# Kernel optimization log

Measured on AMD Instinct MI355X. Metric: run time of the kernel, lower is better.

The kernel has to match this reference:

```python
import jax, jax.numpy as jnp
import numpy as np

EMB = 8
HID = 64
B = 1000
T = 512
N = (B * T) // 5  # events per source; sources partition the (batch,time) grid

_KEYS = ["ccba", "cdtx", "cust", "dp", "remit"]
_NUMS = {"ccba": 8, "cdtx": 1, "cust": 1, "dp": 2, "remit": 1}
_CATS = {"ccba": 0, "cdtx": 2, "cust": 3, "dp": 8, "remit": 1}
_VOCAB = {"ccba": 0, "cdtx": 179, "cust": 37, "dp": 435, "remit": 5}


def setup_inputs() -> dict:
    ks = iter(jax.random.split(jax.random.key(0), 64))
    rng = np.random.default_rng(0)
    chunks = np.split(rng.permutation(B * T), 5)
    d = {}
    for k5, ch in zip(_KEYS, chunks):
        d[k5 + "_num"] = jax.random.normal(next(ks), (N, _NUMS[k5]), jnp.float32)
        if _CATS[k5] > 0:
            d[k5 + "_cat"] = jax.random.randint(next(ks), (N, _CATS[k5]), 0, _VOCAB[k5])
            d[k5 + "_tab"] = jax.random.normal(next(ks), (_VOCAB[k5], EMB), jnp.float32) * 0.1
        d[k5 + "_bi"] = jnp.asarray(ch // T, jnp.int32)
        d[k5 + "_ti"] = jnp.asarray(ch % T, jnp.int32)
        in_dim = _CATS[k5] * EMB + _NUMS[k5]
        d[k5 + "_W"] = jax.random.normal(next(ks), (in_dim, HID), jnp.float32) * np.float32(1.0 / np.sqrt(in_dim))
        d[k5 + "_b"] = jnp.zeros((HID,), jnp.float32)
    # LSTM: 2 layers x 2 directions, hidden 64, proj_size 1 -> layer1 input is 2
    for l, insz in [(0, HID), (1, 2)]:
        d[f"Wih{l}"] = jax.random.normal(next(ks), (2, 4 * HID, insz), jnp.float32) * 0.05
        d[f"Whh{l}"] = jax.random.normal(next(ks), (2, 4 * HID, 1), jnp.float32) * 0.05
        d[f"Whr{l}"] = jax.random.normal(next(ks), (2, 1, HID), jnp.float32) * 0.05
        d[f"bih{l}"] = jnp.zeros((2, 4 * HID), jnp.float32)
        d[f"bhh{l}"] = jnp.zeros((2, 4 * HID), jnp.float32)
    d["length"] = T
    d["batch_size"] = B
    return d


def _embed(num, cat, tab, W, b):
    # FeatureEmbedder: concat(categorical embeddings, numeric) -> Linear(hidden)
    x = num if cat is None else jnp.concatenate([tab[cat].reshape(cat.shape[0], -1), num], axis=-1)
    return x @ W + b


def _lstm_dir(x, Wih, Whh, Whr, bih, bhh, reverse):
    Bx = x.shape[0]
    H = Whr.shape[1]
    p = Whr.shape[0]
    bias = bih + bhh

    def step(carry, xt):
        h, c = carry  # h: [B,p] projected hidden, c: [B,H] cell
        g = xt @ Wih.T + h @ Whh.T + bias
        i, f, gg, o = jnp.split(g, 4, axis=-1)  # PyTorch gate order i,f,g,o
        c = jax.nn.sigmoid(f) * c + jax.nn.sigmoid(i) * jnp.tanh(gg)
        h = (jax.nn.sigmoid(o) * jnp.tanh(c)) @ Whr.T  # proj_size projection
        return (h, c), h

    init = (jnp.zeros((Bx, p), x.dtype), jnp.zeros((Bx, H), x.dtype))
    _, ys = jax.lax.scan(step, init, jnp.swapaxes(x, 0, 1), reverse=reverse)
    return jnp.swapaxes(ys, 0, 1)  # [B,T,p]


def _bilstm(x, Wih, Whh, Whr, bih, bhh):
    fwd = _lstm_dir(x, Wih[0], Whh[0], Whr[0], bih[0], bhh[0], False)
    bwd = _lstm_dir(x, Wih[1], Whh[1], Whr[1], bih[1], bhh[1], True)
    return jnp.concatenate([fwd, bwd], axis=-1)


def _forward(a):
    feat = jnp.zeros((a["batch_size"], a["length"], HID), jnp.float32)
    for k5 in _KEYS:
        v = _embed(a[k5 + "_num"], a.get(k5 + "_cat"), a.get(k5 + "_tab"), a[k5 + "_W"], a[k5 + "_b"])
        feat = feat.at[a[k5 + "_bi"], a[k5 + "_ti"]].set(v)  # scatter-assemble padded tensor
    h = _bilstm(feat, a["Wih0"], a["Whh0"], a["Whr0"], a["bih0"], a["bhh0"])
    h = _bilstm(h, a["Wih1"], a["Whh1"], a["Whr1"], a["bih1"], a["bhh1"])
    return h.mean(axis=2)  # [B,T]


def reference(ccba_num, ccba_bi, ccba_ti, ccba_W, ccba_b,
              cdtx_num, cdtx_cat, cdtx_tab, cdtx_bi, cdtx_ti, cdtx_W, cdtx_b,
              cust_num, cust_cat, cust_tab, cust_bi, cust_ti, cust_W, cust_b,
              dp_num, dp_cat, dp_tab, dp_bi, dp_ti, dp_W, dp_b,
              remit_num, remit_cat, remit_tab, remit_bi, remit_ti, remit_W, remit_b,
              Wih0, Whh0, Whr0, bih0, bhh0, Wih1, Whh1, Whr1, bih1, bhh1,
              length, batch_size):
    return _forward(dict(locals()))
```

## Files before the change

### kernel.cpp

```cpp
#include <hip/hip_runtime.h>
#include <cstdint>
#include <cstddef>

#define TLEN 512
#define BATCH 1000
#define NEV 102400
#define HID 64

__device__ __forceinline__ float fast_rcp(float x) {
#if __has_builtin(__builtin_amdgcn_rcpf)
    return __builtin_amdgcn_rcpf(x);
#else
    return 1.0f / x;
#endif
}
__device__ __forceinline__ float sigm(float x) { return fast_rcp(1.0f + __expf(-x)); }
__device__ __forceinline__ float tanh_f(float x) { return fmaf(2.0f, sigm(2.0f * x), -1.0f); }


__global__ __launch_bounds__(512) void compose_kernel(
    const float* __restrict__ W0, const float* __restrict__ B0,
    const float* __restrict__ W1, const float* __restrict__ B1,
    const float* __restrict__ W2, const float* __restrict__ B2,
    const float* __restrict__ W3, const float* __restrict__ B3,
    const float* __restrict__ W4, const float* __restrict__ B4,
    const float* __restrict__ Wih, const float* __restrict__ bih,
    const float* __restrict__ bhh, float* __restrict__ wp)
{
    const int col = threadIdx.x;
    const int row = blockIdx.x;
    const float* srcW; const float* srcB; int base, IND;
    if (row < 9)        { srcW = W0; srcB = B0; base = 0;   IND = 8;  }
    else if (row < 27)  { srcW = W1; srcB = B1; base = 9;   IND = 17; }
    else if (row < 53)  { srcW = W2; srcB = B2; base = 27;  IND = 25; }
    else if (row < 120) { srcW = W3; srcB = B3; base = 53;  IND = 66; }
    else                { srcW = W4; srcB = B4; base = 120; IND = 9;  }
    const int j = row - base;
    const float* xrow = (j < IND) ? (srcW + (size_t)j * 64) : srcB;
    const float* wr = Wih + (size_t)col * 64;
    float acc = 0.0f;
#pragma unroll
    for (int h2 = 0; h2 < 64; ++h2) acc = fmaf(xrow[h2], wr[h2], acc);
    if (j == IND) acc += bih[col] + bhh[col];
    wp[(size_t)row * 512 + col] = acc;
}

template<int NNUM, int NCAT>
__global__ __launch_bounds__(512) void project_kernel(
    const float* __restrict__ num, const int* __restrict__ cat,
    const float* __restrict__ tab, const int* __restrict__ bi,
    const int* __restrict__ ti, const float* __restrict__ wp,
    float* __restrict__ gpre)
{
    constexpr int IND = NCAT * 8 + NNUM;
    const int col = threadIdx.x;
    float wcol[IND];
#pragma unroll
    for (int j = 0; j < IND; ++j) wcol[j] = wp[(size_t)j * 512 + col];
    const float bcol = wp[(size_t)IND * 512 + col];

    for (int ev = blockIdx.x; ev < NEV; ev += gridDim.x) {
        const int pos = bi[ev] * TLEN + ti[ev];
        float acc = bcol;
#pragma unroll
        for (int c0 = 0; c0 < NCAT; ++c0) {
            const int idx = cat[ev * NCAT + c0];
            const float* tr = tab + (size_t)idx * 8;
#pragma unroll
            for (int u = 0; u < 8; ++u)
                acc = fmaf(tr[u], wcol[c0 * 8 + u], acc);
        }
#pragma unroll
        for (int u = 0; u < NNUM; ++u)
            acc = fmaf(num[(size_t)ev * NNUM + u], wcol[NCAT * 8 + u], acc);
        gpre[(size_t)pos * 512 + col] = acc;
    }
}

__global__ __launch_bounds__(256) void rec0_kernel(
    const float* __restrict__ gpre, const float* __restrict__ Whh,
    const float* __restrict__ Whr, float* __restrict__ h0)
{
    const int wv = threadIdx.x >> 6, lane = threadIdx.x & 63;
    const int p = blockIdx.x * 4 + wv;
    const int b = p >> 1, dir = p & 1;

    float whh4[4];
#pragma unroll
    for (int k = 0; k < 4; ++k) whh4[k] = Whh[dir * 256 + k * 64 + lane];
    const float whr = Whr[dir * HID + lane];

    const float* gb = gpre + (size_t)dir * 256 + lane;
    float* h0p = h0 + (size_t)b * TLEN * 2 + dir;

    auto addr = [&](int t) -> const float* {
        int tc = t < TLEN ? t : TLEN - 1;
        int tt = dir ? (TLEN - 1 - tc) : tc;
        return gb + ((size_t)(b * TLEN + tt)) * 512;
    };

    float A[4], B[4];
    {
        const float* pa = addr(0); const float* pb = addr(1);
#pragma unroll
        for (int k = 0; k < 4; ++k) { A[k] = pa[k * 64]; B[k] = pb[k * 64]; }
    }
    float h = 0.0f, c = 0.0f;

    for (int t = 0; t < TLEN; t += 2) {
        float C[4], D[4];
        const float* pc = addr(t + 2); const float* pd = addr(t + 3);
#pragma unroll
        for (int k = 0; k < 4; ++k) { C[k] = pc[k * 64]; D[k] = pd[k * 64]; }

        {
            float gi = fmaf(whh4[0], h, A[0]);
            float gf = fmaf(whh4[1], h, A[1]);
            float gg = fmaf(whh4[2], h, A[2]);
            float go = fmaf(whh4[3], h, A[3]);
            c = sigm(gf) * c + sigm(gi) * tanh_f(gg);
            float pp = sigm(go) * tanh_f(c) * whr;
#pragma unroll
            for (int off = 1; off < 64; off <<= 1) pp += __shfl_xor(pp, off, 64);
            h = pp;
            int tt = dir ? (TLEN - 1 - t) : t;
            if (lane == 0) h0p[(size_t)tt * 2] = h;
        }
        {
            float gi = fmaf(whh4[0], h, B[0]);
            float gf = fmaf(whh4[1], h, B[1]);
            float gg = fmaf(whh4[2], h, B[2]);
            float go = fmaf(whh4[3], h, B[3]);
            c = sigm(gf) * c + sigm(gi) * tanh_f(gg);
            float pp = sigm(go) * tanh_f(c) * whr;
#pragma unroll
            for (int off = 1; off < 64; off <<= 1) pp += __shfl_xor(pp, off, 64);
            h = pp;
            int tt = dir ? (TLEN - 2 - t) : (t + 1);
            if (lane == 0) h0p[(size_t)tt * 2] = h;
        }
#pragma unroll
        for (int k = 0; k < 4; ++k) { A[k] = C[k]; B[k] = D[k]; }
    }
}

__global__ __launch_bounds__(256) void lstm1_kernel(
    const float* __restrict__ h0, const float* __restrict__ Wih,
    const float* __restrict__ Whh, const float* __restrict__ Whr,
    const float* __restrict__ bih, const float* __restrict__ bhh,
    float* __restrict__ h1)
{
    int w = threadIdx.x >> 6, lane = threadIdx.x & 63;
    int p = blockIdx.x * 4 + w;
    int b = p >> 1, dir = p & 1;

    float wi0[4], wi1[4], whh[4], bias[4];
#pragma unroll
    for (int k = 0; k < 4; ++k) {
        int r = k * 64 + lane;
        wi0[k] = Wih[(size_t)(dir * 256 + r) * 2 + 0];
        wi1[k] = Wih[(size_t)(dir * 256 + r) * 2 + 1];
        whh[k] = Whh[dir * 256 + r];
        bias[k] = bih[dir * 256 + r] + bhh[dir * 256 + r];
    }
    float whr = Whr[dir * HID + lane];
    float h = 0.0f, c = 0.0f;
    const float* hb = h0 + (size_t)b * TLEN * 2;

    auto xat = [&](int t) -> float2 {
        int tc = t < TLEN ? t : TLEN - 1;
        int tt = dir ? (TLEN - 1 - tc) : tc;
        return *(const float2*)(hb + (size_t)tt * 2);
    };

    float2 xA = xat(0), xB = xat(1);
    for (int t = 0; t < TLEN; t += 2) {
        float2 xC = xat(t + 2), xD = xat(t + 3);
        {
            float g[4];
#pragma unroll
            for (int k = 0; k < 4; ++k)
                g[k] = fmaf(whh[k], h, fmaf(wi1[k], xA.y, fmaf(wi0[k], xA.x, bias[k])));
            c = sigm(g[1]) * c + sigm(g[0]) * tanh_f(g[2]);
            float pp = sigm(g[3]) * tanh_f(c) * whr;
#pragma unroll
            for (int off = 1; off < 64; off <<= 1) pp += __shfl_xor(pp, off, 64);
            h = pp;
            int tt = dir ? (TLEN - 1 - t) : t;
            if (lane == 0) h1[((size_t)b * TLEN + tt) * 2 + dir] = h;
        }
        {
            float g[4];
#pragma unroll
            for (int k = 0; k < 4; ++k)
                g[k] = fmaf(whh[k], h, fmaf(wi1[k], xB.y, fmaf(wi0[k], xB.x, bias[k])));
            c = sigm(g[1]) * c + sigm(g[0]) * tanh_f(g[2]);
            float pp = sigm(g[3]) * tanh_f(c) * whr;
#pragma unroll
            for (int off = 1; off < 64; off <<= 1) pp += __shfl_xor(pp, off, 64);
            h = pp;
            int tt = dir ? (TLEN - 2 - t) : (t + 1);
            if (lane == 0) h1[((size_t)b * TLEN + tt) * 2 + dir] = h;
        }
        xA = xC; xB = xD;
    }
}

__global__ __launch_bounds__(256) void mean_kernel(
    const float2* __restrict__ h1, float* __restrict__ out)
{
    int i = blockIdx.x * 256 + threadIdx.x;
    if (i < BATCH * TLEN) {
        float2 v = h1[i];
        out[i] = 0.5f * (v.x + v.y);
    }
}

__global__ __launch_bounds__(256) void embed_kernel(
    const float* __restrict__ num, const int* __restrict__ cat,
    const float* __restrict__ tab, const int* __restrict__ bi,
    const int* __restrict__ ti, const float* __restrict__ W,
    const float* __restrict__ bvec, float* __restrict__ feat,
    int n_num, int n_cat)
{
    int e = blockIdx.x * 4 + (threadIdx.x >> 6);
    int hh = threadIdx.x & 63;
    if (e >= NEV) return;
    float acc = bvec[hh];
    int j = 0;
    for (int c = 0; c < n_cat; ++c) {
        int idx = cat[e * n_cat + c];
        const float* trow = tab + (size_t)idx * 8;
#pragma unroll
        for (int u = 0; u < 8; ++u)
            acc = fmaf(trow[u], W[(j + u) * HID + hh], acc);
        j += 8;
    }
    for (int u = 0; u < n_num; ++u)
        acc = fmaf(num[(size_t)e * n_num + u], W[(j + u) * HID + hh], acc);
    int pos = bi[e] * TLEN + ti[e];
    feat[(size_t)pos * HID + hh] = acc;
}

__global__ __launch_bounds__(256, 2) void lstm0_kernel(
    const float* __restrict__ feat, const float* __restrict__ Wih,
    const float* __restrict__ Whh, const float* __restrict__ Whr,
    const float* __restrict__ bih, const float* __restrict__ bhh,
    float* __restrict__ h0)
{
    const int b0 = blockIdx.x * 4;
    const int dir = blockIdx.y;
    const int tid = threadIdx.x, lane = tid & 63, wv = tid >> 6;

    const float* wrow = Wih + (size_t)(dir * 256 + tid) * HID;
    float4 w[16];
#pragma unroll
    for (int i = 0; i < 16; ++i) w[i] = ((const float4*)wrow)[i];
    const float whh = Whh[dir * 256 + tid];
    const float bias = bih[dir * 256 + tid] + bhh[dir * 256 + tid];
    const float whr = Whr[dir * HID + lane];

    __shared__ float4 featb[2][4][16];
    __shared__ float gbuf[4][256];
    __shared__ __align__(16) float hbuf[4];

    float c = 0.0f;
    const float* fb = feat + (size_t)(b0 + wv) * TLEN * HID;
    float* h0b = h0 + ((size_t)(b0 + wv) * TLEN) * 2 + dir;

    const int t0 = dir ? (TLEN - 1) : 0;
    ((float*)featb[0][wv])[lane] = fb[(size_t)t0 * HID + lane];
    if (tid < 4) hbuf[tid] = 0.0f;
    __syncthreads();

    for (int t = 0; t < TLEN; ++t) {
        const int buf = t & 1;
        const int tt = dir ? (TLEN - 1 - t) : t;
        float nf = 0.0f;
        const int tn = dir ? (TLEN - 2 - t) : (t + 1);
        const bool pf = (t < TLEN - 1);
        if (pf) nf = fb[(size_t)tn * HID + lane];
        const float4 hp = *(const float4*)hbuf;
        float a0 = fmaf(whh, hp.x, bias);
        float a1 = fmaf(whh, hp.y, bias);
        float a2 = fmaf(whh, hp.z, bias);
        float a3 = fmaf(whh, hp.w, bias);
#pragma unroll
        for (int i = 0; i < 16; ++i) {
            float4 f0 = featb[buf][0][i];
            float4 f1 = featb[buf][1][i];
            float4 f2 = featb[buf][2][i];
            float4 f3 = featb[buf][3][i];
            a0 = fmaf(f0.x, w[i].x, a0); a0 = fmaf(f0.y, w[i].y, a0);
            a0 = fmaf(f0.z, w[i].z, a0); a0 = fmaf(f0.w, w[i].w, a0);
            a1 = fmaf(f1.x, w[i].x, a1); a1 = fmaf(f1.y, w[i].y, a1);
            a1 = fmaf(f1.z, w[i].z, a1); a1 = fmaf(f1.w, w[i].w, a1);
            a2 = fmaf(f2.x, w[i].x, a2); a2 = fmaf(f2.y, w[i].y, a2);
            a2 = fmaf(f2.z, w[i].z, a2); a2 = fmaf(f2.w, w[i].w, a2);
            a3 = fmaf(f3.x, w[i].x, a3); a3 = fmaf(f3.y, w[i].y, a3);
            a3 = fmaf(f3.z, w[i].z, a3); a3 = fmaf(f3.w, w[i].w, a3);
        }
        gbuf[0][tid] = a0;
        gbuf[1][tid] = a1;
        gbuf[2][tid] = a2;
        gbuf[3][tid] = a3;
        if (pf) ((float*)featb[1 - buf][wv])[lane] = nf;
        __syncthreads();
        const float gi = gbuf[wv][lane];
        const float gf = gbuf[wv][64 + lane];
        const float gg = gbuf[wv][128 + lane];
        const float go = gbuf[wv][192 + lane];
        c = sigm(gf) * c + sigm(gi) * tanh_f(gg);
        float p = sigm(go) * tanh_f(c) * whr;
#pragma unroll
        for (int off = 1; off < 64; off <<= 1) p += __shfl_xor(p, off, 64);
        if (lane == 0) {
            hbuf[wv] = p;
            h0b[(size_t)tt * 2] = p;
        }
        __syncthreads();
    }
}

extern "C" void kernel_launch(void* const* d_in, const int* in_sizes, int n_in,
                              void* d_out, int out_size, void* d_ws, size_t ws_size,
                              hipStream_t stream)
{
    const float* ccba_num = (const float*)d_in[0];
    const int*   ccba_bi  = (const int*)d_in[1];
    const int*   ccba_ti  = (const int*)d_in[2];
    const float* ccba_W   = (const float*)d_in[3];
    const float* ccba_b   = (const float*)d_in[4];
    const float* cdtx_num = (const float*)d_in[5];
    const int*   cdtx_cat = (const int*)d_in[6];
    const float* cdtx_tab = (const float*)d_in[7];
    const int*   cdtx_bi  = (const int*)d_in[8];
    const int*   cdtx_ti  = (const int*)d_in[9];
    const float* cdtx_W   = (const float*)d_in[10];
    const float* cdtx_b   = (const float*)d_in[11];
    const float* cust_num = (const float*)d_in[12];
    const int*   cust_cat = (const int*)d_in[13];
    const float* cust_tab = (const float*)d_in[14];
    const int*   cust_bi  = (const int*)d_in[15];
    const int*   cust_ti  = (const int*)d_in[16];
    const float* cust_W   = (const float*)d_in[17];
    const float* cust_b   = (const float*)d_in[18];
    const float* dp_num   = (const float*)d_in[19];
    const int*   dp_cat   = (const int*)d_in[20];
    const float* dp_tab   = (const float*)d_in[21];
    const int*   dp_bi    = (const int*)d_in[22];
    const int*   dp_ti    = (const int*)d_in[23];
    const float* dp_W     = (const float*)d_in[24];
    const float* dp_b     = (const float*)d_in[25];
    const float* remit_num = (const float*)d_in[26];
    const int*   remit_cat = (const int*)d_in[27];
    const float* remit_tab = (const float*)d_in[28];
    const int*   remit_bi  = (const int*)d_in[29];
    const int*   remit_ti  = (const int*)d_in[30];
    const float* remit_W   = (const float*)d_in[31];
    const float* remit_b   = (const float*)d_in[32];
    const float* Wih0 = (const float*)d_in[33];
    const float* Whh0 = (const float*)d_in[34];
    const float* Whr0 = (const float*)d_in[35];
    const float* bih0 = (const float*)d_in[36];
    const float* bhh0 = (const float*)d_in[37];
    const float* Wih1 = (const float*)d_in[38];
    const float* Whh1 = (const float*)d_in[39];
    const float* Whr1 = (const float*)d_in[40];
    const float* bih1 = (const float*)d_in[41];
    const float* bhh1 = (const float*)d_in[42];

    float* out = (float*)d_out;
    dim3 blk(256);

    const size_t GPRE_BYTES = (size_t)512000 * 512 * 4;
    const size_t H0_OFF = GPRE_BYTES;
    const size_t H1_OFF = H0_OFF + 4096000;
    const size_t WP_OFF = H1_OFF + 4096000;
    const size_t NEED   = WP_OFF + 130 * 512 * 4;

    if (ws_size >= NEED) {
        char* ws = (char*)d_ws;
        float* gpre = (float*)ws;
        float* h0   = (float*)(ws + H0_OFF);
        float* h1   = (float*)(ws + H1_OFF);
        float* wp   = (float*)(ws + WP_OFF);

        compose_kernel<<<130, 512, 0, stream>>>(
            ccba_W, ccba_b, cdtx_W, cdtx_b, cust_W, cust_b,
            dp_W, dp_b, remit_W, remit_b, Wih0, bih0, bhh0, wp);

        project_kernel<8, 0><<<512, 512, 0, stream>>>(ccba_num, nullptr, nullptr, ccba_bi, ccba_ti, wp + (size_t)0 * 512, gpre);
        project_kernel<1, 2><<<512, 512, 0, stream>>>(cdtx_num, cdtx_cat, cdtx_tab, cdtx_bi, cdtx_ti, wp + (size_t)9 * 512, gpre);
        project_kernel<1, 3><<<512, 512, 0, stream>>>(cust_num, cust_cat, cust_tab, cust_bi, cust_ti, wp + (size_t)27 * 512, gpre);
        project_kernel<2, 8><<<512, 512, 0, stream>>>(dp_num, dp_cat, dp_tab, dp_bi, dp_ti, wp + (size_t)53 * 512, gpre);
        project_kernel<1, 1><<<512, 512, 0, stream>>>(remit_num, remit_cat, remit_tab, remit_bi, remit_ti, wp + (size_t)120 * 512, gpre);

        rec0_kernel<<<500, blk, 0, stream>>>(gpre, Whh0, Whr0, h0);
        lstm1_kernel<<<500, blk, 0, stream>>>(h0, Wih1, Whh1, Whr1, bih1, bhh1, h1);
        mean_kernel<<<(BATCH * TLEN + 255) / 256, blk, 0, stream>>>((const float2*)h1, out);
    } else {
        char* ws = (char*)d_ws;
        float* feat = (float*)ws;
        float* h0   = (float*)(ws + 131072000);
        float* h1   = (float*)(ws + 135168000);
        int eg = (NEV + 3) / 4;
        embed_kernel<<<eg, blk, 0, stream>>>(ccba_num, nullptr, nullptr, ccba_bi, ccba_ti, ccba_W, ccba_b, feat, 8, 0);
        embed_kernel<<<eg, blk, 0, stream>>>(cdtx_num, cdtx_cat, cdtx_tab, cdtx_bi, cdtx_ti, cdtx_W, cdtx_b, feat, 1, 2);
        embed_kernel<<<eg, blk, 0, stream>>>(cust_num, cust_cat, cust_tab, cust_bi, cust_ti, cust_W, cust_b, feat, 1, 3);
        embed_kernel<<<eg, blk, 0, stream>>>(dp_num, dp_cat, dp_tab, dp_bi, dp_ti, dp_W, dp_b, feat, 2, 8);
        embed_kernel<<<eg, blk, 0, stream>>>(remit_num, remit_cat, remit_tab, remit_bi, remit_ti, remit_W, remit_b, feat, 1, 1);
        lstm0_kernel<<<dim3(BATCH / 4, 2), blk, 0, stream>>>(feat, Wih0, Whh0, Whr0, bih0, bhh0, h0);
        lstm1_kernel<<<500, blk, 0, stream>>>(h0, Wih1, Whh1, Whr1, bih1, bhh1, h1);
        mean_kernel<<<(BATCH * TLEN + 255) / 256, blk, 0, stream>>>((const float2*)h1, out);
    }
}
```

Measured before the change: 1.548 ms.

## Chunk layer-0 gate projection over time and replace shuffle reduction with DPP

Drops the two workspace-size-dependent paths and always runs layer 0 in time chunks sized to fit the available workspace. Each chunk's gate pre-activations are written per direction in a compact, step-contiguous layout, using a per-block queue that keeps only events whose time index falls in the chunk. The recurrent kernel carries h and c between chunks through small state buffers. The wave-wide sum now uses DPP row operations plus readlane instead of xor shuffles. This trades more launches and repeated filtering of all events per chunk for a smaller gate buffer and better locality.

```diff
diff --git a/kernel.cpp b/kernel.cpp
--- a/kernel.cpp
+++ b/kernel.cpp
@@ -4,7 +4,7 @@
 
 #define TLEN 512
 #define BATCH 1000
-#define NEV 102400
+#define NEVS 102400
 #define HID 64
 
 __device__ __forceinline__ float fast_rcp(float x) {
@@ -17,6 +17,21 @@
 __device__ __forceinline__ float sigm(float x) { return fast_rcp(1.0f + __expf(-x)); }
 __device__ __forceinline__ float tanh_f(float x) { return fmaf(2.0f, sigm(2.0f * x), -1.0f); }
 
+__device__ __forceinline__ float wave_sum_bcast(float x) {
+#if __has_builtin(__builtin_amdgcn_update_dpp) && __has_builtin(__builtin_amdgcn_readlane)
+    x += __int_as_float(__builtin_amdgcn_update_dpp(0, __float_as_int(x), 0x111, 0xf, 0xf, true));
+    x += __int_as_float(__builtin_amdgcn_update_dpp(0, __float_as_int(x), 0x112, 0xf, 0xf, true));
+    x += __int_as_float(__builtin_amdgcn_update_dpp(0, __float_as_int(x), 0x114, 0xf, 0xf, true));
+    x += __int_as_float(__builtin_amdgcn_update_dpp(0, __float_as_int(x), 0x118, 0xf, 0xf, true));
+    x += __int_as_float(__builtin_amdgcn_update_dpp(0, __float_as_int(x), 0x142, 0xa, 0xf, true));
+    x += __int_as_float(__builtin_amdgcn_update_dpp(0, __float_as_int(x), 0x143, 0xc, 0xf, true));
+    return __int_as_float(__builtin_amdgcn_readlane(__float_as_int(x), 63));
+#else
+#pragma unroll
+    for (int off = 1; off < 64; off <<= 1) x += __shfl_xor(x, off, 64);
+    return x;
+#endif
+}
 
 __global__ __launch_bounds__(512) void compose_kernel(
     const float* __restrict__ W0, const float* __restrict__ B0,
@@ -46,40 +61,112 @@
 }
 
 template<int NNUM, int NCAT>
-__global__ __launch_bounds__(512) void project_kernel(
+__device__ __forceinline__ void project_src(
     const float* __restrict__ num, const int* __restrict__ cat,
     const float* __restrict__ tab, const int* __restrict__ bi,
-    const int* __restrict__ ti, const float* __restrict__ wp,
-    float* __restrict__ gpre)
+    const int* __restrict__ ti, const float* __restrict__ wrows,
+    float* __restrict__ gdst, int dir, int lo, int hi, int tcm,
+    int* qcnt, int* queue)
 {
     constexpr int IND = NCAT * 8 + NNUM;
-    const int col = threadIdx.x;
+    const int tid = threadIdx.x;
+    const int col = dir * 256 + tid;
     float wcol[IND];
 #pragma unroll
-    for (int j = 0; j < IND; ++j) wcol[j] = wp[(size_t)j * 512 + col];
-    const float bcol = wp[(size_t)IND * 512 + col];
-
-    for (int ev = blockIdx.x; ev < NEV; ev += gridDim.x) {
-        const int pos = bi[ev] * TLEN + ti[ev];
-        float acc = bcol;
-#pragma unroll
-        for (int c0 = 0; c0 < NCAT; ++c0) {
-            const int idx = cat[ev * NCAT + c0];
-            const float* tr = tab + (size_t)idx * 8;
-#pragma unroll
-            for (int u = 0; u < 8; ++u)
-                acc = fmaf(tr[u], wcol[c0 * 8 + u], acc);
+    for (int j = 0; j < IND; ++j) wcol[j] = wrows[(size_t)j * 512 + col];
+    const float bcol = wrows[(size_t)IND * 512 + col];
+
+    const int S = gridDim.x;
+    const int per = (NEVS + S - 1) / S;
+    const int e0 = blockIdx.x * per;
+    const int e1 = (e0 + per < NEVS) ? (e0 + per) : NEVS;
+
+    for (int base = e0; base < e1; base += 256) {
+        if (tid == 0) *qcnt = 0;
+        __syncthreads();
+        {
+            const int ev = base + tid;
+            if (ev < e1) {
+                const int t = ti[ev];
+                if (t >= lo && t < hi) {
+                    const int s = atomicAdd(qcnt, 1);
+                    queue[s] = ev;
+                }
+            }
         }
-#pragma unroll
-        for (int u = 0; u < NNUM; ++u)
-            acc = fmaf(num[(size_t)ev * NNUM + u], wcol[NCAT * 8 + u], acc);
-        gpre[(size_t)pos * 512 + col] = acc;
-    }
-}
-
-__global__ __launch_bounds__(256) void rec0_kernel(
-    const float* __restrict__ gpre, const float* __restrict__ Whh,
-    const float* __restrict__ Whr, float* __restrict__ h0)
+        __syncthreads();
+        const int n = *qcnt;
+        for (int i = 0; i < n; i += 2) {
+            const int eA = __builtin_amdgcn_readfirstlane(queue[i]);
+            const bool two = (i + 1 < n);
+            const int eB = two ? __builtin_amdgcn_readfirstlane(queue[i + 1]) : eA;
+            float accA = bcol, accB = bcol;
+#pragma unroll
+            for (int c0 = 0; c0 < NCAT; ++c0) {
+                const int ia = cat[eA * NCAT + c0];
+                const int ib = cat[eB * NCAT + c0];
+                const float* ta = tab + (size_t)ia * 8;
+                const float* tb = tab + (size_t)ib * 8;
+#pragma unroll
+                for (int u = 0; u < 8; ++u) {
+                    accA = fmaf(ta[u], wcol[c0 * 8 + u], accA);
+                    accB = fmaf(tb[u], wcol[c0 * 8 + u], accB);
+                }
+            }
+#pragma unroll
+            for (int u = 0; u < NNUM; ++u) {
+                accA = fmaf(num[(size_t)eA * NNUM + u], wcol[NCAT * 8 + u], accA);
+                accB = fmaf(num[(size_t)eB * NNUM + u], wcol[NCAT * 8 + u], accB);
+            }
+            {
+                const int tA = ti[eA], pA = bi[eA];
+                const int lA = dir ? (hi - 1 - tA) : (tA - lo);
+                gdst[((size_t)pA * tcm + lA) * 256 + tid] = accA;
+            }
+            if (two) {
+                const int tB = ti[eB], pB = bi[eB];
+                const int lB = dir ? (hi - 1 - tB) : (tB - lo);
+                gdst[((size_t)pB * tcm + lB) * 256 + tid] = accB;
+            }
+        }
+        __syncthreads();
+    }
+}
+
+__global__ __launch_bounds__(256) void project_chunk_kernel(
+    const float* __restrict__ ccba_num, const int* __restrict__ ccba_bi, const int* __restrict__ ccba_ti,
+    const float* __restrict__ cdtx_num, const int* __restrict__ cdtx_cat, const float* __restrict__ cdtx_tab,
+    const int* __restrict__ cdtx_bi, const int* __restrict__ cdtx_ti,
+    const float* __restrict__ cust_num, const int* __restrict__ cust_cat, const float* __restrict__ cust_tab,
+    const int* __restrict__ cust_bi, const int* __restrict__ cust_ti,
+    const float* __restrict__ dp_num, const int* __restrict__ dp_cat, const float* __restrict__ dp_tab,
+    const int* __restrict__ dp_bi, const int* __restrict__ dp_ti,
+    const float* __restrict__ remit_num, const int* __restrict__ remit_cat, const float* __restrict__ remit_tab,
+    const int* __restrict__ remit_bi, const int* __restrict__ remit_ti,
+    const float* __restrict__ wp, float* __restrict__ gf, float* __restrict__ gb,
+    int f0, int len, int tcm)
+{
+    __shared__ int qcnt;
+    __shared__ int queue[256];
+    const int dir = blockIdx.y & 1;
+    const int src = blockIdx.y >> 1;
+    const int lo = dir ? (TLEN - f0 - len) : f0;
+    const int hi = lo + len;
+    float* gdst = dir ? gb : gf;
+    switch (src) {
+        case 0: project_src<8, 0>(ccba_num, nullptr, nullptr, ccba_bi, ccba_ti, wp + 0 * 512,   gdst, dir, lo, hi, tcm, &qcnt, queue); break;
+        case 1: project_src<1, 2>(cdtx_num, cdtx_cat, cdtx_tab, cdtx_bi, cdtx_ti, wp + 9 * 512,  gdst, dir, lo, hi, tcm, &qcnt, queue); break;
+        case 2: project_src<1, 3>(cust_num, cust_cat, cust_tab, cust_bi, cust_ti, wp + 27 * 512, gdst, dir, lo, hi, tcm, &qcnt, queue); break;
+        case 3: project_src<2, 8>(dp_num,   dp_cat,   dp_tab,   dp_bi,   dp_ti,   wp + 53 * 512, gdst, dir, lo, hi, tcm, &qcnt, queue); break;
+        default: project_src<1, 1>(remit_num, remit_cat, remit_tab, remit_bi, remit_ti, wp + 120 * 512, gdst, dir, lo, hi, tcm, &qcnt, queue); break;
+    }
+}
+
+__global__ __launch_bounds__(256) void rec_chunk_kernel(
+    const float* __restrict__ gf, const float* __restrict__ gb,
+    const float* __restrict__ Whh, const float* __restrict__ Whr,
+    float* __restrict__ h0, float* __restrict__ hs, float* __restrict__ cs,
+    int f0, int len, int tcm, int first)
 {
     const int wv = threadIdx.x >> 6, lane = threadIdx.x & 63;
     const int p = blockIdx.x * 4 + wv;
@@ -90,58 +177,37 @@
     for (int k = 0; k < 4; ++k) whh4[k] = Whh[dir * 256 + k * 64 + lane];
     const float whr = Whr[dir * HID + lane];
 
-    const float* gb = gpre + (size_t)dir * 256 + lane;
+    const float* g = (dir ? gb : gf) + (size_t)b * tcm * 256 + lane;
     float* h0p = h0 + (size_t)b * TLEN * 2 + dir;
 
-    auto addr = [&](int t) -> const float* {
-        int tc = t < TLEN ? t : TLEN - 1;
-        int tt = dir ? (TLEN - 1 - tc) : tc;
-        return gb + ((size_t)(b * TLEN + tt)) * 512;
-    };
-
-    float A[4], B[4];
-    {
-        const float* pa = addr(0); const float* pb = addr(1);
-#pragma unroll
-        for (int k = 0; k < 4; ++k) { A[k] = pa[k * 64]; B[k] = pb[k * 64]; }
-    }
-    float h = 0.0f, c = 0.0f;
-
-    for (int t = 0; t < TLEN; t += 2) {
-        float C[4], D[4];
-        const float* pc = addr(t + 2); const float* pd = addr(t + 3);
-#pragma unroll
-        for (int k = 0; k < 4; ++k) { C[k] = pc[k * 64]; D[k] = pd[k * 64]; }
-
-        {
-            float gi = fmaf(whh4[0], h, A[0]);
-            float gf = fmaf(whh4[1], h, A[1]);
-            float gg = fmaf(whh4[2], h, A[2]);
-            float go = fmaf(whh4[3], h, A[3]);
-            c = sigm(gf) * c + sigm(gi) * tanh_f(gg);
-            float pp = sigm(go) * tanh_f(c) * whr;
-#pragma unroll
-            for (int off = 1; off < 64; off <<= 1) pp += __shfl_xor(pp, off, 64);
-            h = pp;
-            int tt = dir ? (TLEN - 1 - t) : t;
-            if (lane == 0) h0p[(size_t)tt * 2] = h;
-        }
-        {
-            float gi = fmaf(whh4[0], h, B[0]);
-            float gf = fmaf(whh4[1], h, B[1]);
-            float gg = fmaf(whh4[2], h, B[2]);
-            float go = fmaf(whh4[3], h, B[3]);
-            c = sigm(gf) * c + sigm(gi) * tanh_f(gg);
-            float pp = sigm(go) * tanh_f(c) * whr;
-#pragma unroll
-            for (int off = 1; off < 64; off <<= 1) pp += __shfl_xor(pp, off, 64);
-            h = pp;
-            int tt = dir ? (TLEN - 2 - t) : (t + 1);
-            if (lane == 0) h0p[(size_t)tt * 2] = h;
-        }
-#pragma unroll
-        for (int k = 0; k < 4; ++k) { A[k] = C[k]; B[k] = D[k]; }
-    }
+    float h, c;
+    if (first) { h = 0.0f; c = 0.0f; }
+    else       { h = hs[p]; c = cs[(size_t)p * 64 + lane]; }
+
+    float A[4];
+#pragma unroll
+    for (int k = 0; k < 4; ++k) A[k] = g[k * 64];
+
+    for (int s = 0; s < len; ++s) {
+        float Nx[4];
+        const int sn = (s + 1 < len) ? (s + 1) : s;
+        const float* gn = g + (size_t)sn * 256;
+#pragma unroll
+        for (int k = 0; k < 4; ++k) Nx[k] = gn[k * 64];
+
+        const float gi = fmaf(whh4[0], h, A[0]);
+        const float gfv = fmaf(whh4[1], h, A[1]);
+        const float gg = fmaf(whh4[2], h, A[2]);
+        const float go = fmaf(whh4[3], h, A[3]);
+        c = sigm(gfv) * c + sigm(gi) * tanh_f(gg);
+        h = wave_sum_bcast(sigm(go) * tanh_f(c) * whr);
+        const int t_out = dir ? (TLEN - 1 - f0 - s) : (f0 + s);
+        if (lane == 0) h0p[(size_t)t_out * 2] = h;
+#pragma unroll
+        for (int k = 0; k < 4; ++k) A[k] = Nx[k];
+    }
+    if (lane == 0) hs[p] = h;
+    cs[(size_t)p * 64 + lane] = c;
 }
 
 __global__ __launch_bounds__(256) void lstm1_kernel(
@@ -182,10 +248,7 @@
             for (int k = 0; k < 4; ++k)
                 g[k] = fmaf(whh[k], h, fmaf(wi1[k], xA.y, fmaf(wi0[k], xA.x, bias[k])));
             c = sigm(g[1]) * c + sigm(g[0]) * tanh_f(g[2]);
-            float pp = sigm(g[3]) * tanh_f(c) * whr;
-#pragma unroll
-            for (int off = 1; off < 64; off <<= 1) pp += __shfl_xor(pp, off, 64);
-            h = pp;
+            h = wave_sum_bcast(sigm(g[3]) * tanh_f(c) * whr);
             int tt = dir ? (TLEN - 1 - t) : t;
             if (lane == 0) h1[((size_t)b * TLEN + tt) * 2 + dir] = h;
         }
@@ -195,10 +258,7 @@
             for (int k = 0; k < 4; ++k)
                 g[k] = fmaf(whh[k], h, fmaf(wi1[k], xB.y, fmaf(wi0[k], xB.x, bias[k])));
             c = sigm(g[1]) * c + sigm(g[0]) * tanh_f(g[2]);
-            float pp = sigm(g[3]) * tanh_f(c) * whr;
-#pragma unroll
-            for (int off = 1; off < 64; off <<= 1) pp += __shfl_xor(pp, off, 64);
-            h = pp;
+            h = wave_sum_bcast(sigm(g[3]) * tanh_f(c) * whr);
             int tt = dir ? (TLEN - 2 - t) : (t + 1);
             if (lane == 0) h1[((size_t)b * TLEN + tt) * 2 + dir] = h;
         }
@@ -213,112 +273,6 @@
     if (i < BATCH * TLEN) {
         float2 v = h1[i];
         out[i] = 0.5f * (v.x + v.y);
-    }
-}
-
-__global__ __launch_bounds__(256) void embed_kernel(
-    const float* __restrict__ num, const int* __restrict__ cat,
-    const float* __restrict__ tab, const int* __restrict__ bi,
-    const int* __restrict__ ti, const float* __restrict__ W,
-    const float* __restrict__ bvec, float* __restrict__ feat,
-    int n_num, int n_cat)
-{
-    int e = blockIdx.x * 4 + (threadIdx.x >> 6);
-    int hh = threadIdx.x & 63;
-    if (e >= NEV) return;
-    float acc = bvec[hh];
-    int j = 0;
-    for (int c = 0; c < n_cat; ++c) {
-        int idx = cat[e * n_cat + c];
-        const float* trow = tab + (size_t)idx * 8;
-#pragma unroll
-        for (int u = 0; u < 8; ++u)
-            acc = fmaf(trow[u], W[(j + u) * HID + hh], acc);
-        j += 8;
-    }
-    for (int u = 0; u < n_num; ++u)
-        acc = fmaf(num[(size_t)e * n_num + u], W[(j + u) * HID + hh], acc);
-    int pos = bi[e] * TLEN + ti[e];
-    feat[(size_t)pos * HID + hh] = acc;
-}
-
-__global__ __launch_bounds__(256, 2) void lstm0_kernel(
-    const float* __restrict__ feat, const float* __restrict__ Wih,
-    const float* __restrict__ Whh, const float* __restrict__ Whr,
-    const float* __restrict__ bih, const float* __restrict__ bhh,
-    float* __restrict__ h0)
-{
-    const int b0 = blockIdx.x * 4;
-    const int dir = blockIdx.y;
-    const int tid = threadIdx.x, lane = tid & 63, wv = tid >> 6;
-
-    const float* wrow = Wih + (size_t)(dir * 256 + tid) * HID;
-    float4 w[16];
-#pragma unroll
-    for (int i = 0; i < 16; ++i) w[i] = ((const float4*)wrow)[i];
-    const float whh = Whh[dir * 256 + tid];
-    const float bias = bih[dir * 256 + tid] + bhh[dir * 256 + tid];
-    const float whr = Whr[dir * HID + lane];
-
-    __shared__ float4 featb[2][4][16];
-    __shared__ float gbuf[4][256];
-    __shared__ __align__(16) float hbuf[4];
-
-    float c = 0.0f;
-    const float* fb = feat + (size_t)(b0 + wv) * TLEN * HID;
-    float* h0b = h0 + ((size_t)(b0 + wv) * TLEN) * 2 + dir;
-
-    const int t0 = dir ? (TLEN - 1) : 0;
-    ((float*)featb[0][wv])[lane] = fb[(size_t)t0 * HID + lane];
-    if (tid < 4) hbuf[tid] = 0.0f;
-    __syncthreads();
-
-    for (int t = 0; t < TLEN; ++t) {
-        const int buf = t & 1;
-        const int tt = dir ? (TLEN - 1 - t) : t;
-        float nf = 0.0f;
-        const int tn = dir ? (TLEN - 2 - t) : (t + 1);
-        const bool pf = (t < TLEN - 1);
-        if (pf) nf = fb[(size_t)tn * HID + lane];
-        const float4 hp = *(const float4*)hbuf;
-        float a0 = fmaf(whh, hp.x, bias);
-        float a1 = fmaf(whh, hp.y, bias);
-        float a2 = fmaf(whh, hp.z, bias);
-        float a3 = fmaf(whh, hp.w, bias);
-#pragma unroll
-        for (int i = 0; i < 16; ++i) {
-            float4 f0 = featb[buf][0][i];
-            float4 f1 = featb[buf][1][i];
-            float4 f2 = featb[buf][2][i];
-            float4 f3 = featb[buf][3][i];
-            a0 = fmaf(f0.x, w[i].x, a0); a0 = fmaf(f0.y, w[i].y, a0);
-            a0 = fmaf(f0.z, w[i].z, a0); a0 = fmaf(f0.w, w[i].w, a0);
-            a1 = fmaf(f1.x, w[i].x, a1); a1 = fmaf(f1.y, w[i].y, a1);
-            a1 = fmaf(f1.z, w[i].z, a1); a1 = fmaf(f1.w, w[i].w, a1);
-            a2 = fmaf(f2.x, w[i].x, a2); a2 = fmaf(f2.y, w[i].y, a2);
-            a2 = fmaf(f2.z, w[i].z, a2); a2 = fmaf(f2.w, w[i].w, a2);
-            a3 = fmaf(f3.x, w[i].x, a3); a3 = fmaf(f3.y, w[i].y, a3);
-            a3 = fmaf(f3.z, w[i].z, a3); a3 = fmaf(f3.w, w[i].w, a3);
-        }
-        gbuf[0][tid] = a0;
-        gbuf[1][tid] = a1;
-        gbuf[2][tid] = a2;
-        gbuf[3][tid] = a3;
-        if (pf) ((float*)featb[1 - buf][wv])[lane] = nf;
-        __syncthreads();
-        const float gi = gbuf[wv][lane];
-        const float gf = gbuf[wv][64 + lane];
-        const float gg = gbuf[wv][128 + lane];
-        const float go = gbuf[wv][192 + lane];
-        c = sigm(gf) * c + sigm(gi) * tanh_f(gg);
-        float p = sigm(go) * tanh_f(c) * whr;
-#pragma unroll
-        for (int off = 1; off < 64; off <<= 1) p += __shfl_xor(p, off, 64);
-        if (lane == 0) {
-            hbuf[wv] = p;
-            h0b[(size_t)tt * 2] = p;
-        }
-        __syncthreads();
     }
 }
 
@@ -371,47 +325,42 @@
     const float* bhh1 = (const float*)d_in[42];
 
     float* out = (float*)d_out;
-    dim3 blk(256);
-
-    const size_t GPRE_BYTES = (size_t)512000 * 512 * 4;
-    const size_t H0_OFF = GPRE_BYTES;
-    const size_t H1_OFF = H0_OFF + 4096000;
-    const size_t WP_OFF = H1_OFF + 4096000;
-    const size_t NEED   = WP_OFF + 130 * 512 * 4;
-
-    if (ws_size >= NEED) {
-        char* ws = (char*)d_ws;
-        float* gpre = (float*)ws;
-        float* h0   = (float*)(ws + H0_OFF);
-        float* h1   = (float*)(ws + H1_OFF);
-        float* wp   = (float*)(ws + WP_OFF);
-
-        compose_kernel<<<130, 512, 0, stream>>>(
-            ccba_W, ccba_b, cdtx_W, cdtx_b, cust_W, cust_b,
-            dp_W, dp_b, remit_W, remit_b, Wih0, bih0, bhh0, wp);
-
-        project_kernel<8, 0><<<512, 512, 0, stream>>>(ccba_num, nullptr, nullptr, ccba_bi, ccba_ti, wp + (size_t)0 * 512, gpre);
-        project_kernel<1, 2><<<512, 512, 0, stream>>>(cdtx_num, cdtx_cat, cdtx_tab, cdtx_bi, cdtx_ti, wp + (size_t)9 * 512, gpre);
-        project_kernel<1, 3><<<512, 512, 0, stream>>>(cust_num, cust_cat, cust_tab, cust_bi, cust_ti, wp + (size_t)27 * 512, gpre);
-        project_kernel<2, 8><<<512, 512, 0, stream>>>(dp_num, dp_cat, dp_tab, dp_bi, dp_ti, wp + (size_t)53 * 512, gpre);
-        project_kernel<1, 1><<<512, 512, 0, stream>>>(remit_num, remit_cat, remit_tab, remit_bi, remit_ti, wp + (size_t)120 * 512, gpre);
-
-        rec0_kernel<<<500, blk, 0, stream>>>(gpre, Whh0, Whr0, h0);
-        lstm1_kernel<<<500, blk, 0, stream>>>(h0, Wih1, Whh1, Whr1, bih1, bhh1, h1);
-        mean_kernel<<<(BATCH * TLEN + 255) / 256, blk, 0, stream>>>((const float2*)h1, out);
-    } else {
-        char* ws = (char*)d_ws;
-        float* feat = (float*)ws;
-        float* h0   = (float*)(ws + 131072000);
-        float* h1   = (float*)(ws + 135168000);
-        int eg = (NEV + 3) / 4;
-        embed_kernel<<<eg, blk, 0, stream>>>(ccba_num, nullptr, nullptr, ccba_bi, ccba_ti, ccba_W, ccba_b, feat, 8, 0);
-        embed_kernel<<<eg, blk, 0, stream>>>(cdtx_num, cdtx_cat, cdtx_tab, cdtx_bi, cdtx_ti, cdtx_W, cdtx_b, feat, 1, 2);
-        embed_kernel<<<eg, blk, 0, stream>>>(cust_num, cust_cat, cust_tab, cust_bi, cust_ti, cust_W, cust_b, feat, 1, 3);
-        embed_kernel<<<eg, blk, 0, stream>>>(dp_num, dp_cat, dp_tab, dp_bi, dp_ti, dp_W, dp_b, feat, 2, 8);
-        embed_kernel<<<eg, blk, 0, stream>>>(remit_num, remit_cat, remit_tab, remit_bi, remit_ti, remit_W, remit_b, feat, 1, 1);
-        lstm0_kernel<<<dim3(BATCH / 4, 2), blk, 0, stream>>>(feat, Wih0, Whh0, Whr0, bih0, bhh0, h0);
-        lstm1_kernel<<<500, blk, 0, stream>>>(h0, Wih1, Whh1, Whr1, bih1, bhh1, h1);
-        mean_kernel<<<(BATCH * TLEN + 255) / 256, blk, 0, stream>>>((const float2*)h1, out);
-    }
-}
+
+    const size_t FIXED = 4096000ull + 4096000ull + 266240ull + 8000ull + 512000ull;
+    size_t avail = (ws_size > FIXED) ? (ws_size - FIXED) : 0;
+    int tcm = (int)(avail / 2048000ull);
+    if (tcm < 1) tcm = 1;
+    if (tcm > TLEN) tcm = TLEN;
+
+    char* ws = (char*)d_ws;
+    const size_t gfB = (size_t)tcm * 1024000ull;
+    float* gf = (float*)ws;
+    float* gb = (float*)(ws + gfB);
+    float* h0 = (float*)(ws + 2 * gfB);
+    float* h1 = (float*)(ws + 2 * gfB + 4096000ull);
+    float* wp = (float*)(ws + 2 * gfB + 8192000ull);
+    float* hs = (float*)(ws + 2 * gfB + 8192000ull + 266240ull);
+    float* cs = (float*)(ws + 2 * gfB + 8192000ull + 266240ull + 8000ull);
+
+    compose_kernel<<<130, 512, 0, stream>>>(
+        ccba_W, ccba_b, cdtx_W, cdtx_b, cust_W, cust_b,
+        dp_W, dp_b, remit_W, remit_b, Wih0, bih0, bhh0, wp);
+
+    int first = 1;
+    for (int f0 = 0; f0 < TLEN; f0 += tcm) {
+        const int len = (TLEN - f0 < tcm) ? (TLEN - f0) : tcm;
+        project_chunk_kernel<<<dim3(256, 10), 256, 0, stream>>>(
+            ccba_num, ccba_bi, ccba_ti,
+            cdtx_num, cdtx_cat, cdtx_tab, cdtx_bi, cdtx_ti,
+            cust_num, cust_cat, cust_tab, cust_bi, cust_ti,
+            dp_num, dp_cat, dp_tab, dp_bi, dp_ti,
+            remit_num, remit_cat, remit_tab, remit_bi, remit_ti,
+            wp, gf, gb, f0, len, tcm);
+        rec_chunk_kernel<<<500, 256, 0, stream>>>(
+            gf, gb, Whh0, Whr0, h0, hs, cs, f0, len, tcm, first);
+        first = 0;
+    }
+
+    lstm1_kernel<<<500, 256, 0, stream>>>(h0, Wih1, Whh1, Whr1, bih1, bhh1, h1);
+    mean_kernel<<<(BATCH * TLEN + 255) / 256, 256, 0, stream>>>((const float2*)h1, out);
+}
```

Result: faster. 1.471 ms (-4.9%).
